# Optimization experiments

Hardware: AMD Instinct MI355X
Metric: run time of the kernel (lower is better)

Reference implementation:

```python
import jax, jax.numpy as jnp
import numpy as np

D_MODEL = 1024
NUM_HEADS = 16
D_KEY = D_MODEL // NUM_HEADS


def setup_inputs() -> dict:
    key = jax.random.key(0)
    ks = jax.random.split(key, 9)
    s = 1.0 / np.sqrt(D_MODEL)
    inp = {
        "x": jax.random.normal(ks[0], (4, 2048, D_MODEL), dtype=jnp.float32),
        "Wq": jax.random.uniform(ks[1], (D_MODEL, D_MODEL), jnp.float32, -s, s),
        "bq": jax.random.uniform(ks[2], (D_MODEL,), jnp.float32, -s, s),
        "Wk": jax.random.uniform(ks[3], (D_MODEL, D_MODEL), jnp.float32, -s, s),
        "bk": jax.random.uniform(ks[4], (D_MODEL,), jnp.float32, -s, s),
        "Wv": jax.random.uniform(ks[5], (D_MODEL, D_MODEL), jnp.float32, -s, s),
        "bv": jax.random.uniform(ks[6], (D_MODEL,), jnp.float32, -s, s),
        "Wo": jax.random.uniform(ks[7], (D_MODEL, D_MODEL), jnp.float32, -s, s),
        "bo": jax.random.uniform(ks[8], (D_MODEL,), jnp.float32, -s, s),
    }
    return inp


def reference(x, Wq, bq, Wk, bk, Wv, bv, Wo, bo):
    B, S, D = x.shape
    H, Dk = NUM_HEADS, D_KEY
    # QKV projections (torch Linear: x @ W.T + b; here W stored as [in,out])
    q = (x @ Wq + bq).reshape(B, S, H, Dk).transpose(0, 2, 1, 3)  # [B,H,S,Dk]
    k = (x @ Wk + bk).reshape(B, S, H, Dk).transpose(0, 2, 1, 3)
    v = (x @ Wv + bv).reshape(B, S, H, Dk).transpose(0, 2, 1, 3)
    logits = jnp.einsum("bhqd,bhkd->bhqk", q, k) / jnp.sqrt(jnp.float32(Dk))
    causal = jnp.triu(jnp.ones((S, S), dtype=bool), k=1)  # True above diagonal
    logits = jnp.where(causal, -jnp.inf, logits)
    attn = jax.nn.softmax(logits, axis=-1)
    out = jnp.einsum("bhqk,bhkd->bhqd", attn, v)  # [B,H,S,Dk]
    out = out.transpose(0, 2, 1, 3).reshape(B, S, D)
    return out @ Wo + bo
```

## Files before the change

### kernel.cpp

```cpp
#include <hip/hip_runtime.h>
#include <hip/hip_bf16.h>

#define DEVI __device__ __forceinline__

typedef __attribute__((ext_vector_type(8))) __bf16 bf16x8;
typedef __attribute__((ext_vector_type(4))) float f32x4;
typedef __attribute__((ext_vector_type(16))) float f32x16;
typedef __attribute__((ext_vector_type(8))) unsigned short ushort8;
typedef __attribute__((ext_vector_type(4))) int i32x4;

constexpr int D_MODEL = 1024;
constexpr int NHEAD   = 16;
constexpr int SEQ     = 2048;
constexpr int BATCH   = 4;
constexpr int MTOK    = BATCH * SEQ;

DEVI unsigned short f2bf(float x) {
  __hip_bfloat16 h = __float2bfloat16(x);
  return __builtin_bit_cast(unsigned short, h);
}

DEVI bf16x8 ld_bf8(const unsigned short* p) {
  ushort8 u = *reinterpret_cast<const ushort8*>(p);
  return __builtin_bit_cast(bf16x8, u);
}

DEVI void gload_lds16(const void* g, void* l) {
  __builtin_amdgcn_global_load_lds(
      (const __attribute__((address_space(1))) void*)g,
      (__attribute__((address_space(3))) void*)l, 16, 0, 0);
}

DEVI int cvtpk(float a, float b) {
  int r;
  asm("v_cvt_pk_bf16_f32 %0, %1, %2" : "=v"(r) : "v"(a), "v"(b));
  return r;
}
DEVI void pswap(int& a, int& b) {
  asm volatile("v_permlane32_swap_b32 %0, %1" : "+v"(a), "+v"(b));
}
DEVI float xhalf_sum(float x) { return x + __shfl_xor(x, 32, 64); }

DEVI float tree16sum(const float* p) {
  float a = p[0] + p[1], b = p[2] + p[3], c = p[4] + p[5], d = p[6] + p[7];
  float e = p[8] + p[9], f = p[10] + p[11], g = p[12] + p[13], h = p[14] + p[15];
  a += b; c += d; e += f; g += h;
  return (a + c) + (e + g);
}
DEVI bf16x8 mk_frag(const float* p, int off) {
  int w0 = cvtpk(p[off + 0], p[off + 1]);
  int w1 = cvtpk(p[off + 2], p[off + 3]);
  int w2 = cvtpk(p[off + 4], p[off + 5]);
  int w3 = cvtpk(p[off + 6], p[off + 7]);
  pswap(w0, w2);
  pswap(w1, w3);
  i32x4 v{w0, w1, w2, w3};
  return __builtin_bit_cast(bf16x8, v);
}

__global__ void cvt_f32_bf16(const float* __restrict__ in,
                             unsigned short* __restrict__ out, int n) {
  int i = (blockIdx.x * blockDim.x + threadIdx.x) * 4;
  if (i >= n) return;
  float4 v = *reinterpret_cast<const float4*>(in + i);
  ushort4 o;
  o.x = f2bf(v.x); o.y = f2bf(v.y); o.z = f2bf(v.z); o.w = f2bf(v.w);
  *reinterpret_cast<ushort4*>(out + i) = o;
}

__global__ void wt_kernel(const float* __restrict__ Wq, const float* __restrict__ Wk,
                          const float* __restrict__ Wv, const float* __restrict__ Wo,
                          unsigned short* __restrict__ Wtq, unsigned short* __restrict__ Wtk,
                          unsigned short* __restrict__ Wtv, unsigned short* __restrict__ Wto) {
  __shared__ float tile[64][65];
  const int wsel = blockIdx.z;
  const float* W = wsel == 0 ? Wq : wsel == 1 ? Wk : wsel == 2 ? Wv : Wo;
  unsigned short* Wt = wsel == 0 ? Wtq : wsel == 1 ? Wtk : wsel == 2 ? Wtv : Wto;
  const int k0 = blockIdx.x * 64, n0 = blockIdx.y * 64;
  const int tx = threadIdx.x & 63, ty = threadIdx.x >> 6;
  for (int r = ty; r < 64; r += 4)
    tile[r][tx] = W[(size_t)(k0 + r) * D_MODEL + n0 + tx];
  __syncthreads();
  for (int r = ty; r < 64; r += 4)
    Wt[(size_t)(n0 + r) * D_MODEL + k0 + tx] = f2bf(tile[tx][r]);
}

__global__ __launch_bounds__(256) void gemm128(
    const unsigned short* __restrict__ A,
    const unsigned short* __restrict__ Bt,
    const float* __restrict__ bias,
    void* __restrict__ outp, int mode, float scale) {
  constexpr int K = 1024, N = 1024;
  __shared__ __align__(16) unsigned short As[2][128 * 64];
  __shared__ __align__(16) unsigned short Bs[2][128 * 64];
  const int t = threadIdx.x;
  const int w = t >> 6, l = t & 63;
  const int bid2 = ((blockIdx.x & 7) << 6) | (blockIdx.x >> 3);
  const int bm = bid2 >> 3, bn = bid2 & 7;
  const int m0 = bm * 128, n0 = bn * 128;
  const int wm = (w >> 1) * 64, wn = (w & 1) * 64;
  const int lr = l & 15, lg = l >> 4;

  f32x4 acc[4][4] = {};

  auto stage = [&](int kt, int buf) {
    const int k0 = kt * 64;
#pragma unroll
    for (int p = 0; p < 4; ++p) {
      const int seg = p * 4 + w;
      const int row = seg * 8 + (l >> 3);
      const int c = (l & 7) ^ (row & 7);
      gload_lds16(A + (size_t)(m0 + row) * K + k0 + c * 8, &As[buf][seg * 512]);
      gload_lds16(Bt + (size_t)(n0 + row) * K + k0 + c * 8, &Bs[buf][seg * 512]);
    }
  };

  stage(0, 0);
  __syncthreads();

  for (int kt = 0; kt < K / 64; ++kt) {
    const int cur = kt & 1;
    if (kt + 1 < K / 64) stage(kt + 1, cur ^ 1);
#pragma unroll
    for (int ks = 0; ks < 2; ++ks) {
      bf16x8 af[4], bfr[4];
      const int kk = lg + ks * 4;
#pragma unroll
      for (int i = 0; i < 4; ++i) {
        const int rowA = wm + i * 16 + lr;
        af[i] = ld_bf8(&As[cur][rowA * 64 + ((kk ^ (rowA & 7)) * 8)]);
        const int rowB = wn + i * 16 + lr;
        bfr[i] = ld_bf8(&Bs[cur][rowB * 64 + ((kk ^ (rowB & 7)) * 8)]);
      }
#pragma unroll
      for (int mi = 0; mi < 4; ++mi)
#pragma unroll
        for (int ni = 0; ni < 4; ++ni)
          acc[mi][ni] = __builtin_amdgcn_mfma_f32_16x16x32_bf16(
              af[mi], bfr[ni], acc[mi][ni], 0, 0, 0);
    }
    __syncthreads();
  }

#pragma unroll
  for (int ni = 0; ni < 4; ++ni) {
    const int n = n0 + wn + ni * 16 + lr;
    const float bv = bias[n];
#pragma unroll
    for (int mi = 0; mi < 4; ++mi) {
#pragma unroll
      for (int r = 0; r < 4; ++r) {
        const int m = m0 + wm + mi * 16 + lg * 4 + r;
        const float v = (acc[mi][ni][r] + bv) * scale;
        if (mode == 2) {
          ((float*)outp)[(size_t)m * N + n] = v;
        } else {
          const int b = m >> 11, s = m & 2047, h = n >> 6, dk = n & 63;
          unsigned short* o = (unsigned short*)outp;
          if (mode == 0)
            o[(((size_t)(b * NHEAD + h) * SEQ + s) << 6) + dk] = f2bf(v);
          else
            o[(((size_t)(b * NHEAD + h) << 6) + dk) * SEQ + s] = f2bf(v);
        }
      }
    }
  }
}

__global__ __launch_bounds__(256) void attn_kernel(
    const unsigned short* __restrict__ Q,
    const unsigned short* __restrict__ Kt,
    const unsigned short* __restrict__ Vt,
    unsigned short* __restrict__ Oa) {
  __shared__ __align__(16) unsigned short Ks[2][64 * 64];
  __shared__ __align__(16) unsigned short Vs[2][64 * 64];
  const int t = threadIdx.x, w = t >> 6, l = t & 63;
  const int bid = blockIdx.x;
  const int tix = bid >> 6;
  const int tk = tix >> 2, tg = tix & 3;
  const int qt = tk == 0 ? 15 - tg : tk == 1 ? 8 + tg : tk == 2 ? 4 + tg : 3 - tg;
  const int bh = bid & 63;
  const int l31 = l & 31, hi = l >> 5;
  const int jcnt = 2 * qt + 2;
  const int q0w = qt * 128 + w * 32;
  const int qg = q0w + l31;

  const unsigned short* Qb = Q + ((size_t)bh * SEQ + qg) * 64;
  bf16x8 qf[4];
#pragma unroll
  for (int ks = 0; ks < 4; ++ks)
    qf[ks] = ld_bf8(Qb + ks * 16 + hi * 8);

  f32x16 psum = {};
  f32x16 oacc[2] = {};

  auto stage = [&](int jtile, int buf) {
#pragma unroll
    for (int i = 0; i < 2; ++i) {
      const int seg = w * 2 + i;
      const int row = seg * 8 + (l >> 3);
      const int cg = (l & 7) ^ (row & 7);
      gload_lds16(Kt + (((size_t)bh * SEQ + jtile * 64 + row) << 6) + cg * 8,
                  &Ks[buf][seg * 512]);
      gload_lds16(Vt + ((size_t)bh * 64 + row) * SEQ + jtile * 64 + cg * 8,
                  &Vs[buf][seg * 512]);
    }
  };

  stage(0, 0);
  __syncthreads();

  for (int jt = 0; jt < jcnt; ++jt) {
    const int cur = jt & 1;
    if (jt + 1 < jcnt) stage(jt + 1, cur ^ 1);
    const int j0 = jt * 64;
    const bool active = (j0 <= q0w + 31);
    if (active) {
      const bool live1 = (j0 < q0w);
      const bool maskT = (j0 + 32 >= q0w);

      f32x16 s0 = {}, s1 = {};
      __builtin_amdgcn_s_setprio(1);
#pragma unroll
      for (int ks = 0; ks < 4; ++ks) {
        bf16x8 kf = ld_bf8(&Ks[cur][l31 * 64 + ((((ks << 1) | hi) ^ (l31 & 7)) << 3)]);
        s0 = __builtin_amdgcn_mfma_f32_32x32x16_bf16(kf, qf[ks], s0, 0, 0, 0);
      }
      if (live1) {
#pragma unroll
        for (int ks = 0; ks < 4; ++ks) {
          const int r1 = 32 + l31;
          bf16x8 kf = ld_bf8(&Ks[cur][r1 * 64 + ((((ks << 1) | hi) ^ (r1 & 7)) << 3)]);
          s1 = __builtin_amdgcn_mfma_f32_32x32x16_bf16(kf, qf[ks], s1, 0, 0, 0);
        }
      }
      __builtin_amdgcn_s_setprio(0);

      float p0[16];
      if (maskT) {
#pragma unroll
        for (int r = 0; r < 16; ++r) {
          const int key = j0 + (r & 3) + ((r >> 2) << 3) + (hi << 2);
          p0[r] = (key > qg) ? 0.f : exp2f(s0[r]);
        }
      } else {
#pragma unroll
        for (int r = 0; r < 16; ++r) p0[r] = exp2f(s0[r]);
      }
#pragma unroll
      for (int r = 0; r < 16; ++r) psum[r] += p0[r];

      __builtin_amdgcn_s_setprio(1);
#pragma unroll
      for (int ks = 0; ks < 2; ++ks) {
        bf16x8 pf = mk_frag(p0, ks * 8);
#pragma unroll
        for (int dt = 0; dt < 2; ++dt) {
          const int rv = dt * 32 + l31;
          bf16x8 vf = ld_bf8(&Vs[cur][rv * 64 + ((((ks << 1) | hi) ^ (rv & 7)) << 3)]);
          oacc[dt] = __builtin_amdgcn_mfma_f32_32x32x16_bf16(vf, pf, oacc[dt], 0, 0, 0);
        }
      }
      __builtin_amdgcn_s_setprio(0);

      if (live1) {
        float p1[16];
        if (maskT) {
#pragma unroll
          for (int r = 0; r < 16; ++r) {
            const int key = j0 + 32 + (r & 3) + ((r >> 2) << 3) + (hi << 2);
            p1[r] = (key > qg) ? 0.f : exp2f(s1[r]);
          }
        } else {
#pragma unroll
          for (int r = 0; r < 16; ++r) p1[r] = exp2f(s1[r]);
        }
#pragma unroll
        for (int r = 0; r < 16; ++r) psum[r] += p1[r];
        __builtin_amdgcn_s_setprio(1);
#pragma unroll
        for (int ks = 0; ks < 2; ++ks) {
          bf16x8 pf = mk_frag(p1, ks * 8);
#pragma unroll
          for (int dt = 0; dt < 2; ++dt) {
            const int rv = dt * 32 + l31;
            bf16x8 vf = ld_bf8(&Vs[cur][rv * 64 + (((((ks + 2) << 1) | hi) ^ (rv & 7)) << 3)]);
            oacc[dt] = __builtin_amdgcn_mfma_f32_32x32x16_bf16(vf, pf, oacc[dt], 0, 0, 0);
          }
        }
        __builtin_amdgcn_s_setprio(0);
      }
    }
    __syncthreads();
  }

  float pa[16];
#pragma unroll
  for (int r = 0; r < 16; ++r) pa[r] = psum[r];
  const float l_ = xhalf_sum(tree16sum(pa));
  const float rinv = 1.f / l_;
  const int b = bh >> 4, h = bh & 15;
  unsigned short* orow = Oa + ((size_t)(b * SEQ) + qg) * D_MODEL + h * 64;
#pragma unroll
  for (int dt = 0; dt < 2; ++dt)
#pragma unroll
    for (int g = 0; g < 4; ++g) {
      const int d = dt * 32 + g * 8 + hi * 4;
      uint2 u;
      u.x = (unsigned)cvtpk(oacc[dt][g * 4 + 0] * rinv, oacc[dt][g * 4 + 1] * rinv);
      u.y = (unsigned)cvtpk(oacc[dt][g * 4 + 2] * rinv, oacc[dt][g * 4 + 3] * rinv);
      *reinterpret_cast<uint2*>(orow + d) = u;
    }
}

extern "C" void kernel_launch(void* const* d_in, const int* in_sizes, int n_in,
                              void* d_out, int out_size, void* d_ws, size_t ws_size,
                              hipStream_t stream) {
  const float* x  = (const float*)d_in[0];
  const float* Wq = (const float*)d_in[1];
  const float* bq = (const float*)d_in[2];
  const float* Wk = (const float*)d_in[3];
  const float* bk = (const float*)d_in[4];
  const float* Wv = (const float*)d_in[5];
  const float* bv = (const float*)d_in[6];
  const float* Wo = (const float*)d_in[7];
  const float* bo = (const float*)d_in[8];

  char* ws = (char*)d_ws;
  unsigned short* xb    = (unsigned short*)(ws + 0);
  unsigned short* attnb = (unsigned short*)(ws + 0);
  unsigned short* wtq   = (unsigned short*)(ws + 16777216);
  unsigned short* wtk   = (unsigned short*)(ws + 18874368);
  unsigned short* wtv   = (unsigned short*)(ws + 20971520);
  unsigned short* wto   = (unsigned short*)(ws + 23068672);
  unsigned short* Qw    = (unsigned short*)(ws + 25165824);
  unsigned short* Kw    = (unsigned short*)(ws + 41943040);
  unsigned short* Vtw   = (unsigned short*)(ws + 58720256);

  cvt_f32_bf16<<<8192, 256, 0, stream>>>(x, xb, MTOK * D_MODEL);
  wt_kernel<<<dim3(16, 16, 4), 256, 0, stream>>>(Wq, Wk, Wv, Wo, wtq, wtk, wtv, wto);

  gemm128<<<512, 256, 0, stream>>>(xb, wtq, bq, (void*)Qw, 0, 0.18033688011112042f);
  gemm128<<<512, 256, 0, stream>>>(xb, wtk, bk, (void*)Kw, 0, 1.0f);
  gemm128<<<512, 256, 0, stream>>>(xb, wtv, bv, (void*)Vtw, 1, 1.0f);

  attn_kernel<<<1024, 256, 0, stream>>>(Qw, Kw, Vtw, attnb);

  gemm128<<<512, 256, 0, stream>>>(attnb, wto, bo, d_out, 2, 1.0f);
}
```

Measured before the change: 202.0 us.

## Widen attention KV tiles to 128 keys and fuse prep kernels into one launch

The attention kernel now stages 128-key K and V tiles per iteration instead of 64, which halves the number of loop iterations and __syncthreads barriers. Each tile is processed as four 32-key sub-steps, with per-lane K offsets precomputed once. The V tile gets a wider 16-chunk XOR swizzle to avoid LDS bank conflicts. Separately, the x fp32-to-bf16 conversion and the weight transpose are merged into one prep kernel to save a launch. The cost is doubled LDS use per block (64 KB vs 32 KB), which may lower occupancy, plus coarser causal tiles that stage some key rows past the diagonal which are then skipped.

Measured after the change: 206.7 us. 2.3% more time.

```diff
diff --git a/kernel.cpp b/kernel.cpp
--- a/kernel.cpp
+++ b/kernel.cpp
@@ -58,24 +58,29 @@
   return __builtin_bit_cast(bf16x8, v);
 }
 
-__global__ void cvt_f32_bf16(const float* __restrict__ in,
-                             unsigned short* __restrict__ out, int n) {
-  int i = (blockIdx.x * blockDim.x + threadIdx.x) * 4;
-  if (i >= n) return;
-  float4 v = *reinterpret_cast<const float4*>(in + i);
-  ushort4 o;
-  o.x = f2bf(v.x); o.y = f2bf(v.y); o.z = f2bf(v.z); o.w = f2bf(v.w);
-  *reinterpret_cast<ushort4*>(out + i) = o;
-}
-
-__global__ void wt_kernel(const float* __restrict__ Wq, const float* __restrict__ Wk,
-                          const float* __restrict__ Wv, const float* __restrict__ Wo,
-                          unsigned short* __restrict__ Wtq, unsigned short* __restrict__ Wtk,
-                          unsigned short* __restrict__ Wtv, unsigned short* __restrict__ Wto) {
+__global__ void prep_kernel(const float* __restrict__ x, unsigned short* __restrict__ xb,
+                            const float* __restrict__ Wq, const float* __restrict__ Wk,
+                            const float* __restrict__ Wv, const float* __restrict__ Wo,
+                            unsigned short* __restrict__ Wtq, unsigned short* __restrict__ Wtk,
+                            unsigned short* __restrict__ Wtv, unsigned short* __restrict__ Wto) {
+  const int z = blockIdx.z;
+  if (z >= 4) {
+    const int bid = (z - 4) * 256 + blockIdx.y * 16 + blockIdx.x;
+    const float4* in4 = reinterpret_cast<const float4*>(x);
+    ushort4* out4 = reinterpret_cast<ushort4*>(xb);
+#pragma unroll
+    for (int j = 0; j < 16; ++j) {
+      const int i4 = bid * 4096 + j * 256 + threadIdx.x;
+      float4 v = in4[i4];
+      ushort4 o;
+      o.x = f2bf(v.x); o.y = f2bf(v.y); o.z = f2bf(v.z); o.w = f2bf(v.w);
+      out4[i4] = o;
+    }
+    return;
+  }
   __shared__ float tile[64][65];
-  const int wsel = blockIdx.z;
-  const float* W = wsel == 0 ? Wq : wsel == 1 ? Wk : wsel == 2 ? Wv : Wo;
-  unsigned short* Wt = wsel == 0 ? Wtq : wsel == 1 ? Wtk : wsel == 2 ? Wtv : Wto;
+  const float* W = z == 0 ? Wq : z == 1 ? Wk : z == 2 ? Wv : Wo;
+  unsigned short* Wt = z == 0 ? Wtq : z == 1 ? Wtk : z == 2 ? Wtv : Wto;
   const int k0 = blockIdx.x * 64, n0 = blockIdx.y * 64;
   const int tx = threadIdx.x & 63, ty = threadIdx.x >> 6;
   for (int r = ty; r < 64; r += 4)
@@ -172,8 +177,8 @@
     const unsigned short* __restrict__ Kt,
     const unsigned short* __restrict__ Vt,
     unsigned short* __restrict__ Oa) {
-  __shared__ __align__(16) unsigned short Ks[2][64 * 64];
-  __shared__ __align__(16) unsigned short Vs[2][64 * 64];
+  __shared__ __align__(16) unsigned short Ks[2][128 * 64];
+  __shared__ __align__(16) unsigned short Vs[2][64 * 128];
   const int t = threadIdx.x, w = t >> 6, l = t & 63;
   const int bid = blockIdx.x;
   const int tix = bid >> 6;
@@ -181,7 +186,7 @@
   const int qt = tk == 0 ? 15 - tg : tk == 1 ? 8 + tg : tk == 2 ? 4 + tg : 3 - tg;
   const int bh = bid & 63;
   const int l31 = l & 31, hi = l >> 5;
-  const int jcnt = 2 * qt + 2;
+  const int jcnt = qt + 1;
   const int q0w = qt * 128 + w * 32;
   const int qg = q0w + l31;
 
@@ -191,19 +196,25 @@
   for (int ks = 0; ks < 4; ++ks)
     qf[ks] = ld_bf8(Qb + ks * 16 + hi * 8);
 
+  int kbase[4];
+#pragma unroll
+  for (int ks = 0; ks < 4; ++ks)
+    kbase[ks] = l31 * 64 + ((((ks << 1) | hi) ^ (l31 & 7)) << 3);
+  const int vx = l31 & 15;
+
   f32x16 psum = {};
   f32x16 oacc[2] = {};
 
   auto stage = [&](int jtile, int buf) {
 #pragma unroll
-    for (int i = 0; i < 2; ++i) {
-      const int seg = w * 2 + i;
-      const int row = seg * 8 + (l >> 3);
-      const int cg = (l & 7) ^ (row & 7);
-      gload_lds16(Kt + (((size_t)bh * SEQ + jtile * 64 + row) << 6) + cg * 8,
-                  &Ks[buf][seg * 512]);
-      gload_lds16(Vt + ((size_t)bh * 64 + row) * SEQ + jtile * 64 + cg * 8,
-                  &Vs[buf][seg * 512]);
+    for (int i = 0; i < 4; ++i) {
+      const int gi = i * 256 + t;
+      const int krow = gi >> 3, kc = (gi & 7) ^ (krow & 7);
+      gload_lds16(Kt + (((size_t)bh * SEQ + jtile * 128 + krow) << 6) + kc * 8,
+                  &Ks[buf][gi * 8]);
+      const int vrow = gi >> 4, vc = (gi & 15) ^ (vrow & 15);
+      gload_lds16(Vt + ((size_t)bh * 64 + vrow) * SEQ + jtile * 128 + vc * 8,
+                  &Vs[buf][gi * 8]);
     }
   };
 
@@ -213,26 +224,19 @@
   for (int jt = 0; jt < jcnt; ++jt) {
     const int cur = jt & 1;
     if (jt + 1 < jcnt) stage(jt + 1, cur ^ 1);
-    const int j0 = jt * 64;
-    const bool active = (j0 <= q0w + 31);
-    if (active) {
-      const bool live1 = (j0 < q0w);
-      const bool maskT = (j0 + 32 >= q0w);
-
-      f32x16 s0 = {}, s1 = {};
+    const int jb = jt * 128;
+#pragma unroll
+    for (int ss = 0; ss < 4; ++ss) {
+      const int j0 = jb + ss * 32;
+      if (j0 > q0w + 31) continue;
+      const bool maskT = (j0 + 31 >= q0w);
+
+      f32x16 s0 = {};
       __builtin_amdgcn_s_setprio(1);
 #pragma unroll
       for (int ks = 0; ks < 4; ++ks) {
-        bf16x8 kf = ld_bf8(&Ks[cur][l31 * 64 + ((((ks << 1) | hi) ^ (l31 & 7)) << 3)]);
+        bf16x8 kf = ld_bf8(&Ks[cur][kbase[ks] + ss * 2048]);
         s0 = __builtin_amdgcn_mfma_f32_32x32x16_bf16(kf, qf[ks], s0, 0, 0, 0);
-      }
-      if (live1) {
-#pragma unroll
-        for (int ks = 0; ks < 4; ++ks) {
-          const int r1 = 32 + l31;
-          bf16x8 kf = ld_bf8(&Ks[cur][r1 * 64 + ((((ks << 1) | hi) ^ (r1 & 7)) << 3)]);
-          s1 = __builtin_amdgcn_mfma_f32_32x32x16_bf16(kf, qf[ks], s1, 0, 0, 0);
-        }
       }
       __builtin_amdgcn_s_setprio(0);
 
@@ -252,44 +256,17 @@
 
       __builtin_amdgcn_s_setprio(1);
 #pragma unroll
-      for (int ks = 0; ks < 2; ++ks) {
-        bf16x8 pf = mk_frag(p0, ks * 8);
+      for (int ks2 = 0; ks2 < 2; ++ks2) {
+        bf16x8 pf = mk_frag(p0, ks2 * 8);
 #pragma unroll
         for (int dt = 0; dt < 2; ++dt) {
           const int rv = dt * 32 + l31;
-          bf16x8 vf = ld_bf8(&Vs[cur][rv * 64 + ((((ks << 1) | hi) ^ (rv & 7)) << 3)]);
+          const int ch = (ss * 4 + ks2 * 2 + hi) ^ vx;
+          bf16x8 vf = ld_bf8(&Vs[cur][rv * 128 + (ch << 3)]);
           oacc[dt] = __builtin_amdgcn_mfma_f32_32x32x16_bf16(vf, pf, oacc[dt], 0, 0, 0);
         }
       }
       __builtin_amdgcn_s_setprio(0);
-
-      if (live1) {
-        float p1[16];
-        if (maskT) {
-#pragma unroll
-          for (int r = 0; r < 16; ++r) {
-            const int key = j0 + 32 + (r & 3) + ((r >> 2) << 3) + (hi << 2);
-            p1[r] = (key > qg) ? 0.f : exp2f(s1[r]);
-          }
-        } else {
-#pragma unroll
-          for (int r = 0; r < 16; ++r) p1[r] = exp2f(s1[r]);
-        }
-#pragma unroll
-        for (int r = 0; r < 16; ++r) psum[r] += p1[r];
-        __builtin_amdgcn_s_setprio(1);
-#pragma unroll
-        for (int ks = 0; ks < 2; ++ks) {
-          bf16x8 pf = mk_frag(p1, ks * 8);
-#pragma unroll
-          for (int dt = 0; dt < 2; ++dt) {
-            const int rv = dt * 32 + l31;
-            bf16x8 vf = ld_bf8(&Vs[cur][rv * 64 + (((((ks + 2) << 1) | hi) ^ (rv & 7)) << 3)]);
-            oacc[dt] = __builtin_amdgcn_mfma_f32_32x32x16_bf16(vf, pf, oacc[dt], 0, 0, 0);
-          }
-        }
-        __builtin_amdgcn_s_setprio(0);
-      }
     }
     __syncthreads();
   }
@@ -337,8 +314,8 @@
   unsigned short* Kw    = (unsigned short*)(ws + 41943040);
   unsigned short* Vtw   = (unsigned short*)(ws + 58720256);
 
-  cvt_f32_bf16<<<8192, 256, 0, stream>>>(x, xb, MTOK * D_MODEL);
-  wt_kernel<<<dim3(16, 16, 4), 256, 0, stream>>>(Wq, Wk, Wv, Wo, wtq, wtk, wtv, wto);
+  prep_kernel<<<dim3(16, 16, 6), 256, 0, stream>>>(x, xb, Wq, Wk, Wv, Wo,
+                                                   wtq, wtk, wtv, wto);
 
   gemm128<<<512, 256, 0, stream>>>(xb, wtq, bq, (void*)Qw, 0, 0.18033688011112042f);
   gemm128<<<512, 256, 0, stream>>>(xb, wtk, bk, (void*)Kw, 0, 1.0f);
```
